# Kernel tuning notes

Hardware: AMD Instinct MI355X
Metric: run time of the kernel (lower is better)

The kernel has to match this reference:

```python
import jax, jax.numpy as jnp
import numpy as np

C = 96
HEADS = 6
WH, WW = 8, 8
N = WH * WW
EPS = 1e-5

def _rel_pos_index(wh, ww):
    ch, cw = np.meshgrid(np.arange(wh), np.arange(ww), indexing='ij')
    cf = np.stack([ch.reshape(-1), cw.reshape(-1)])  # [2, N]
    rel = (cf[:, :, None] - cf[:, None, :]).transpose(1, 2, 0)  # [N, N, 2]
    rel[..., 0] += wh - 1
    rel[..., 1] += ww - 1
    rel[..., 0] *= 2 * ww - 1
    return rel.sum(-1)  # [N, N]

REL_IDX = jnp.asarray(_rel_pos_index(WH, WW).reshape(-1))

def _shift_mask(H, W, wh, ww):
    # standard Swin shifted-window attention mask, values in {0, -100}
    sh, sw = wh // 2, ww // 2
    img = np.zeros((H, W))
    cnt = 0
    for hs in (slice(0, -wh), slice(-wh, -sh), slice(-sh, None)):
        for ws in (slice(0, -ww), slice(-ww, -sw), slice(-sw, None)):
            img[hs, ws] = cnt
            cnt += 1
    mw = img.reshape(H // wh, wh, W // ww, ww).transpose(0, 2, 1, 3).reshape(-1, wh * ww)
    diff = mw[:, None, :] - mw[:, :, None]
    return np.where(diff != 0, -100.0, 0.0).astype(np.float32)  # [nW, N, N]

def _partition(x):
    # [B, C, H, W] -> [B*nW, N, C], window index fastest within batch
    B, Cc, H, W = x.shape
    x = x.transpose(0, 2, 3, 1)
    x = x.reshape(B, H // WH, WH, W // WW, WW, Cc).transpose(0, 1, 3, 2, 4, 5)
    return x.reshape(-1, N, Cc)

def _merge(xw, B, H, W):
    Cc = xw.shape[-1]
    x = xw.reshape(B, H // WH, W // WW, WH, WW, Cc).transpose(0, 1, 3, 2, 4, 5)
    return x.reshape(B, H, W, Cc).transpose(0, 3, 1, 2)

def _ln(x, g, b):
    m = jnp.mean(x, -1, keepdims=True)
    v = jnp.mean((x - m) ** 2, -1, keepdims=True)
    return (x - m) / jnp.sqrt(v + EPS) * g + b

def _wsa(x, wqkv, bqkv, table, wproj, bproj, g, b, mask):
    B_, Nn, Cc = x.shape
    d = Cc // HEADS
    qkv = (x @ wqkv + bqkv).reshape(B_, Nn, 3, HEADS, d).transpose(2, 0, 3, 1, 4)
    q, k, v = qkv[0], qkv[1], qkv[2]
    bias = table[REL_IDX].reshape(Nn, Nn, HEADS).transpose(2, 0, 1)[None]  # [1,H,N,N]
    if mask is not None:
        nW = mask.shape[0]
        bias = bias + jnp.tile(mask, (B_ // nW, 1, 1))[:, None]  # [B_,1,N,N]
    scores = jnp.einsum('bhqd,bhkd->bhqk', q, k) * jnp.float32(1.0 / np.sqrt(d)) + bias
    attn = jax.nn.softmax(scores, axis=-1)
    out = jnp.einsum('bhqk,bhkd->bhqd', attn, v).transpose(0, 2, 1, 3).reshape(B_, Nn, Cc)
    out = out @ wproj + bproj
    return _ln(out + x, g, b)

def _ff(x, w1, b1, w2, b2, g, b):
    y = jax.nn.gelu(x @ w1 + b1, approximate=False) @ w2 + b2
    return _ln(y + x, g, b)

def setup_inputs() -> dict:
    key = jax.random.key(0)
    ks = jax.random.split(key, 20)
    B, H, W = 4, 192, 192
    inp = {'x': jax.random.normal(ks[0], (B, C, H, W), jnp.float32)}
    T = (2 * WH - 1) * (2 * WW - 1)
    def w(k, sh):
        return jax.random.normal(k, sh, jnp.float32) * 0.05
    i = 1
    for p in ('sa1', 'sa2'):
        inp[p + '_wqkv'] = w(ks[i], (C, 3 * C)); i += 1
        inp[p + '_bqkv'] = jnp.zeros((3 * C,), jnp.float32)
        inp[p + '_table'] = w(ks[i], (T, HEADS)); i += 1
        inp[p + '_wproj'] = w(ks[i], (C, C)); i += 1
        inp[p + '_bproj'] = jnp.zeros((C,), jnp.float32)
        inp[p + '_g'] = jnp.ones((C,), jnp.float32)
        inp[p + '_b'] = jnp.zeros((C,), jnp.float32)
    for p in ('ff1', 'ff2'):
        inp[p + '_w1'] = w(ks[i], (C, 2 * C)); i += 1
        inp[p + '_b1'] = jnp.zeros((2 * C,), jnp.float32)
        inp[p + '_w2'] = w(ks[i], (2 * C, C)); i += 1
        inp[p + '_b2'] = jnp.zeros((C,), jnp.float32)
        inp[p + '_g'] = jnp.ones((C,), jnp.float32)
        inp[p + '_b'] = jnp.zeros((C,), jnp.float32)
    return inp

def reference(x, sa1_wqkv, sa1_bqkv, sa1_table, sa1_wproj, sa1_bproj, sa1_g, sa1_b, ff1_w1, ff1_b1, ff1_w2, ff1_b2, ff1_g, ff1_b, sa2_wqkv, sa2_bqkv, sa2_table, sa2_wproj, sa2_bproj, sa2_g, sa2_b, ff2_w1, ff2_b1, ff2_w2, ff2_b2, ff2_g, ff2_b):
    B, Cc, H, W = x.shape
    mask = jnp.asarray(_shift_mask(H, W, WH, WW))
    xw = _partition(x)
    xw = _wsa(xw, sa1_wqkv, sa1_bqkv, sa1_table, sa1_wproj, sa1_bproj, sa1_g, sa1_b, None)
    xw = _ff(xw, ff1_w1, ff1_b1, ff1_w2, ff1_b2, ff1_g, ff1_b)
    x = _merge(xw, B, H, W)
    x = jnp.roll(x, (-(WH // 2), -(WW // 2)), axis=(2, 3))
    xw = _partition(x)
    xw = _wsa(xw, sa2_wqkv, sa2_bqkv, sa2_table, sa2_wproj, sa2_bproj, sa2_g, sa2_b, mask)
    xw = _ff(xw, ff2_w1, ff2_b1, ff2_w2, ff2_b2, ff2_g, ff2_b)
    x = _merge(xw, B, H, W)
    x = jnp.roll(x, (WH // 2, WW // 2), axis=(2, 3))
    return x
```

## Files before the change

kernel.cpp:

```cpp
#include <hip/hip_runtime.h>
#include <hip/hip_bf16.h>

typedef float  f32x4 __attribute__((ext_vector_type(4)));
typedef float  f32x2 __attribute__((ext_vector_type(2)));
typedef short  s16x4 __attribute__((ext_vector_type(4)));
typedef short  s16x8 __attribute__((ext_vector_type(8)));
typedef unsigned short u16;

#define DEVI __device__ __forceinline__
#define MFMA32(A,B,C) __builtin_amdgcn_mfma_f32_16x16x32_bf16(A,B,C,0,0,0)
#define MFMA16(A,B,C) __builtin_amdgcn_mfma_f32_16x16x16bf16_1k(A,B,C,0,0,0)

constexpr int NWD=24, WPI=576, NWIN=2304;
constexpr float LNEPS=1e-5f;
constexpr float LOG2E=1.4426950408889634f;

constexpr size_t PACK_STRIDE = 147456;
constexpr size_t BIAS1_OFF   = 294912;
constexpr size_t BIAS2_OFF   = 393216;
constexpr size_t XT_OFF      = 786432;
constexpr size_t WS1_OFF     = XT_OFF + 28311552;

constexpr int L_X  = 0;
constexpr int L_O  = 13312;
constexpr int L_RED= 26624;
constexpr int L_X2 = 0;
constexpr int L_Y1 = 13312;
constexpr int L_OUT= 13312;
constexpr int WSLICE = 38912;
constexpr int LTOT   = 2*WSLICE;

DEVI u16 f2b(float f){ union{float f;unsigned u;}v; v.f=f; unsigned r=v.u + 0x7FFFu + ((v.u>>16)&1u); return (u16)(r>>16); }
DEVI float b2f(u16 h){ union{unsigned u;float f;}v; v.u=((unsigned)h)<<16; return v.f; }

DEVI s16x4 pack4(f32x4 a){
  union{ __hip_bfloat16 b[4]; s16x4 s; } z;
  #pragma unroll
  for (int i=0;i<4;++i) z.b[i] = __hip_bfloat16(a[i]);
  return z.s;
}

DEVI float fexp2(float x){
#if __has_builtin(__builtin_amdgcn_exp2f)
  return __builtin_amdgcn_exp2f(x);
#else
  return exp2f(x);
#endif
}
DEVI float frcp(float x){
#if __has_builtin(__builtin_amdgcn_rcpf)
  return __builtin_amdgcn_rcpf(x);
#else
  return 1.f/x;
#endif
}

DEVI float gelu_f(float t){
  const float u2 = t*__builtin_fmaf(t*t, 0.1029433f, 2.3022083f);
  return t * frcp(1.f + fexp2(-u2));
}

__global__ void pack_gemm(const float* __restrict__ q1,const float* __restrict__ p1,
                          const float* __restrict__ a1,const float* __restrict__ c1,
                          const float* __restrict__ q2,const float* __restrict__ p2,
                          const float* __restrict__ a2,const float* __restrict__ c2,
                          char* __restrict__ ws){
  const int wv = (blockIdx.x*256 + threadIdx.x)>>6;
  const int lane = threadIdx.x & 63;
  const int stage = wv/144; const int t = wv%144;
  const float* src; int N, off, tl, nkt;
  if (t < 54)      { src = stage? q2:q1; N=288; off=0;      tl=t;     nkt=3; }
  else if (t < 72) { src = stage? p2:p1; N=96;  off=55296;  tl=t-54;  nkt=3; }
  else if (t <108) { src = stage? a2:a1; N=192; off=73728;  tl=t-72;  nkt=3; }
  else             { src = stage? c2:c1; N=96;  off=110592; tl=t-108; nkt=6; }
  const int kt = tl % nkt;
  const int k0 = kt*32 + (lane>>4)*8, n = (tl/nkt)*16 + (lane&15);
  u16 v[8];
  #pragma unroll
  for (int e=0;e<8;++e) v[e] = f2b(src[(k0+e)*N + n]);
  *(s16x8*)(ws + stage*PACK_STRIDE + off + tl*1024 + lane*16) = *(s16x8*)v;
}

__global__ void pack_bias(const float* __restrict__ t1, const float* __restrict__ t2,
                          char* __restrict__ ws){
  const int wv = (blockIdx.x*256 + threadIdx.x)>>6;
  const int lane = threadIdx.x & 63;
  const float* tb; float* dst; int hc=0, wc=0, head, til;
  if (wv < 96){ tb=t1; head=wv>>4; til=wv&15;
                dst=(float*)(ws + BIAS1_OFF + (size_t)((head*16+til)*64+lane)*16); }
  else { int r = wv-96; const int cls = r/96; r %= 96; head=r>>4; til=r&15;
         hc=cls>>1; wc=cls&1; tb=t2;
         dst=(float*)(ws + BIAS2_OFF + cls*98304 + (size_t)((head*16+til)*64+lane)*16); }
  const int mt=til>>2, nt=til&3;
  const int q = nt*16 + (lane&15); const int qi=q>>3, qj=q&7;
  const int rq = (hc?(qi<4?1:2):0)*3 + (wc?(qj<4?1:2):0);
  f32x4 o;
  #pragma unroll
  for (int r4=0;r4<4;++r4){
    const int kk = mt*16 + (lane>>4)*4 + r4; const int ki=kk>>3, kj=kk&7;
    float v = tb[((qi-ki+7)*15 + (qj-kj+7))*6 + head];
    const int rk = (hc?(ki<4?1:2):0)*3 + (wc?(kj<4?1:2):0);
    if (rq != rk) v -= 100.f;
    o[r4]=v*LOG2E;
  }
  *(f32x4*)dst = o;
}

__global__ __launch_bounds__(256) void to_tokens(const float* __restrict__ x, u16* __restrict__ xt){
  __shared__ u16 T[192*100];
  const int b = blockIdx.x/192, h = blockIdx.x%192;
  const int t = threadIdx.x;
  for (int i=t; i<4608; i+=256){
    const int c = i/48, w4 = (i%48)*4;
    const f32x4 v = *(const f32x4*)&x[((size_t)(b*96+c)*192+h)*192 + w4];
    #pragma unroll
    for (int e=0;e<4;++e) T[(w4+e)*100 + c] = f2b(v[e]);
  }
  __syncthreads();
  for (int i=t; i<2304; i+=256){
    const int tok = i/12, c8 = i%12;
    *(s16x8*)&xt[((size_t)(b*192+h)*192+tok)*96 + c8*8] = *(const s16x8*)&T[tok*100 + c8*8];
  }
}

template <int STAGE>
__global__ __launch_bounds__(768, 3) void swin_mfma(
    const u16* __restrict__ srcTok, u16* __restrict__ dstTok,
    const char* __restrict__ pack, const char* __restrict__ biasAll,
    const float* __restrict__ bqkv, const float* __restrict__ bproj,
    const float* __restrict__ g1v, const float* __restrict__ be1v,
    const float* __restrict__ b1v, const float* __restrict__ b2v,
    const float* __restrict__ g2v, const float* __restrict__ be2v)
{
  __shared__ f32x4 LDSv[LTOT/16];
  char* lds = (char*)LDSv;

  const int tid  = threadIdx.x;
  const int lane = tid & 63;
  const int wfl  = __builtin_amdgcn_readfirstlane(tid >> 6);
  const int wh   = wfl/6;
  const int hd   = wfl - 6*wh;
  const int g    = lane >> 4, li = lane & 15;
  const int win  = blockIdx.x*2 + wh;
  const int b    = win / WPI, wrem = win % WPI;
  const int whi  = wrem / NWD, wwi = wrem % NWD;
  char* ldsW     = lds + wh*WSLICE;
  constexpr int SH = (STAGE==2) ? 4 : 0;

  {
    const int wsel = (tid >= 384) ? 1 : 0;
    const int lt   = tid - wsel*384;
    const int winT = blockIdx.x*2 + wsel;
    const int bT   = winT / WPI, wremT = winT % WPI;
    const int h0T  = (wremT/NWD)*8, w0T = (wremT%NWD)*8;
    const int tok = lt/6, ch = lt%6;
    const int hh = (h0T + (tok>>3) + SH)%192, ww = (w0T + (tok&7) + SH)%192;
    const u16* sp = srcTok + ((size_t)(bT*192+hh)*192+ww)*96 + ch*16;
    char* ldsT = lds + wsel*WSLICE;
    *(s16x8*)(ldsT + L_X + tok*208 + ch*32)      = *(const s16x8*)sp;
    *(s16x8*)(ldsT + L_X + tok*208 + ch*32 + 16) = *(const s16x8*)(sp+8);
  }
  __syncthreads();

  s16x4 fq[4], fk[4], fv[4];
  {
    const float SCLQ = 0.25f*LOG2E;
    const f32x4 bqv = *(const f32x4*)(bqkv +      16*hd + 4*g);
    const f32x4 bkv = *(const f32x4*)(bqkv +  96 + 16*hd + 4*g);
    const float bvv = bqkv[192 + 16*hd + li];
    #pragma unroll
    for (int nt=0;nt<4;++nt){
      asm volatile("" ::: "memory");
      f32x4 aq=f32x4{0,0,0,0}, ak=f32x4{0,0,0,0}, av=f32x4{0,0,0,0};
      #pragma unroll
      for (int kt=0;kt<3;++kt){
        const s16x8 wqf = *(const s16x8*)(pack + ((   hd)*3+kt)*1024 + lane*16);
        const s16x8 wkf = *(const s16x8*)(pack + (( 6+hd)*3+kt)*1024 + lane*16);
        const s16x8 wvf = *(const s16x8*)(pack + ((12+hd)*3+kt)*1024 + lane*16);
        const s16x8 xf  = *(const s16x8*)(ldsW + L_X + (16*nt+li)*208 + kt*64 + g*16);
        aq = MFMA32(wqf, xf, aq);
        ak = MFMA32(wkf, xf, ak);
        av = MFMA32(xf, wvf, av);
      }
      f32x4 tq, tk, tv;
      #pragma unroll
      for (int r=0;r<4;++r){
        tq[r] = (aq[r]+bqv[r])*SCLQ;
        tk[r] =  ak[r]+bkv[r];
        tv[r] =  av[r]+bvv;
      }
      fq[nt]=pack4(tq); fk[nt]=pack4(tk); fv[nt]=pack4(tv);
    }
  }

  {
    const char* bb = biasAll;
    if (STAGE==2) bb += (size_t)(((whi==23)?2:0) + ((wwi==23)?1:0)) * 98304;
    #pragma unroll
    for (int nt=0;nt<4;++nt){
      f32x4 sc[4];
      #pragma unroll
      for (int mt=0;mt<4;++mt)
        sc[mt] = *(const f32x4*)(bb + (size_t)((hd*16 + mt*4+nt)*64 + lane)*16);
      #pragma unroll
      for (int mt=0;mt<4;++mt)
        sc[mt] = MFMA16(fk[mt], fq[nt], sc[mt]);
      float m = sc[0][0];
      #pragma unroll
      for (int mt=0;mt<4;++mt)
        #pragma unroll
        for (int r=0;r<4;++r) m = fmaxf(m, sc[mt][r]);
      m = fmaxf(m, __shfl_xor(m,16)); m = fmaxf(m, __shfl_xor(m,32));
      float s = 0.f; s16x4 pb[4];
      #pragma unroll
      for (int mt=0;mt<4;++mt){
        f32x4 pv;
        #pragma unroll
        for (int r=0;r<4;++r){ pv[r] = fexp2(sc[mt][r]-m); s += pv[r]; }
        pb[mt] = pack4(pv);
      }
      s += __shfl_xor(s,16); s += __shfl_xor(s,32);
      const float rs = frcp(s);
      f32x4 oa = f32x4{0,0,0,0};
      #pragma unroll
      for (int kt=0;kt<4;++kt)
        oa = MFMA16(fv[kt], pb[kt], oa);
      f32x4 ov;
      #pragma unroll
      for (int r=0;r<4;++r) ov[r] = oa[r]*rs;
      *(s16x4*)(ldsW + L_O + (16*nt+li)*208 + (16*hd+4*g)*2) = pack4(ov);
    }
  }
  __syncthreads();

  float z[4][4];
  {
    const f32x4 bpv = *(const f32x4*)(bproj + 16*hd + 4*g);
    f32x4 pa[4];
    #pragma unroll
    for (int nt=0;nt<4;++nt) pa[nt]=bpv;
    #pragma unroll
    for (int kt=0;kt<3;++kt){
      const s16x8 wpf = *(const s16x8*)(pack + 55296 + (hd*3+kt)*1024 + lane*16);
      #pragma unroll
      for (int nt=0;nt<4;++nt){
        const s16x8 of = *(const s16x8*)(ldsW + L_O + (16*nt+li)*208 + kt*64 + g*16);
        pa[nt] = MFMA32(wpf, of, pa[nt]);
      }
    }
    #pragma unroll
    for (int nt=0;nt<4;++nt){
      const s16x4 xr = *(const s16x4*)(ldsW + L_X + (16*nt+li)*208 + (16*hd+4*g)*2);
      #pragma unroll
      for (int r=0;r<4;++r) z[nt][r] = pa[nt][r] + b2f((u16)xr[r]);
    }
    #pragma unroll
    for (int nt=0;nt<4;++nt){
      float s1 = z[nt][0]+z[nt][1]+z[nt][2]+z[nt][3];
      float s2 = z[nt][0]*z[nt][0]+z[nt][1]*z[nt][1]+z[nt][2]*z[nt][2]+z[nt][3]*z[nt][3];
      s1 += __shfl_xor(s1,16); s1 += __shfl_xor(s1,32);
      s2 += __shfl_xor(s2,16); s2 += __shfl_xor(s2,32);
      if (lane < 16)
        *(f32x2*)(ldsW + L_RED + (hd*64 + nt*16 + li)*8) = f32x2{s1,s2};
    }
  }
  __syncthreads();
  {
    const f32x4 gv = *(const f32x4*)(g1v + 16*hd + 4*g);
    const f32x4 bv = *(const f32x4*)(be1v + 16*hd + 4*g);
    #pragma unroll
    for (int nt=0;nt<4;++nt){
      float su=0.f, sq=0.f;
      #pragma unroll
      for (int v=0;v<6;++v){
        const f32x2 p = *(const f32x2*)(ldsW + L_RED + (v*64 + nt*16 + li)*8);
        su += p[0]; sq += p[1];
      }
      const float mu = su*(1.f/96.f);
      const float rstd = rsqrtf(sq*(1.f/96.f) - mu*mu + LNEPS);
      f32x4 xo;
      #pragma unroll
      for (int r=0;r<4;++r) xo[r] = (z[nt][r]-mu)*rstd*gv[r] + bv[r];
      *(s16x4*)(ldsW + L_X2 + (16*nt+li)*208 + (16*hd+4*g)*2) = pack4(xo);
    }
  }
  __syncthreads();

  {
    f32x4 ya[2][4];
    #pragma unroll
    for (int jn=0;jn<2;++jn){
      const f32x4 b1f = *(const f32x4*)(b1v + 16*(hd+6*jn) + 4*g);
      #pragma unroll
      for (int nt=0;nt<4;++nt) ya[jn][nt]=b1f;
    }
    #pragma unroll
    for (int kt=0;kt<3;++kt){
      const s16x8 w1f0 = *(const s16x8*)(pack + 73728 + ((hd  )*3+kt)*1024 + lane*16);
      const s16x8 w1f1 = *(const s16x8*)(pack + 73728 + ((hd+6)*3+kt)*1024 + lane*16);
      #pragma unroll
      for (int nt=0;nt<4;++nt){
        const s16x8 xf = *(const s16x8*)(ldsW + L_X2 + (16*nt+li)*208 + kt*64 + g*16);
        ya[0][nt] = MFMA32(w1f0, xf, ya[0][nt]);
        ya[1][nt] = MFMA32(w1f1, xf, ya[1][nt]);
      }
    }
    #pragma unroll
    for (int jn=0;jn<2;++jn)
      #pragma unroll
      for (int nt=0;nt<4;++nt){
        f32x4 yo;
        #pragma unroll
        for (int r=0;r<4;++r) yo[r] = gelu_f(ya[jn][nt][r]);
        *(s16x4*)(ldsW + L_Y1 + (16*nt+li)*400 + (16*(hd+6*jn)+4*g)*2) = pack4(yo);
      }
  }
  __syncthreads();

  float z2[4][4]; float s1v[4], s2v[4];
  {
    const f32x4 b2f4 = *(const f32x4*)(b2v + 16*hd + 4*g);
    f32x4 fa[4];
    #pragma unroll
    for (int nt=0;nt<4;++nt) fa[nt]=b2f4;
    #pragma unroll
    for (int kt=0;kt<6;++kt){
      const s16x8 w2f = *(const s16x8*)(pack + 110592 + (hd*6+kt)*1024 + lane*16);
      #pragma unroll
      for (int nt=0;nt<4;++nt){
        const s16x8 yf = *(const s16x8*)(ldsW + L_Y1 + (16*nt+li)*400 + kt*64 + g*16);
        fa[nt] = MFMA32(w2f, yf, fa[nt]);
      }
    }
    #pragma unroll
    for (int nt=0;nt<4;++nt){
      const s16x4 xr = *(const s16x4*)(ldsW + L_X2 + (16*nt+li)*208 + (16*hd+4*g)*2);
      #pragma unroll
      for (int r=0;r<4;++r) z2[nt][r] = fa[nt][r] + b2f((u16)xr[r]);
    }
    #pragma unroll
    for (int nt=0;nt<4;++nt){
      float s1 = z2[nt][0]+z2[nt][1]+z2[nt][2]+z2[nt][3];
      float s2 = z2[nt][0]*z2[nt][0]+z2[nt][1]*z2[nt][1]+z2[nt][2]*z2[nt][2]+z2[nt][3]*z2[nt][3];
      s1 += __shfl_xor(s1,16); s1 += __shfl_xor(s1,32);
      s2 += __shfl_xor(s2,16); s2 += __shfl_xor(s2,32);
      s1v[nt]=s1; s2v[nt]=s2;
    }
  }
  __syncthreads();
  if (lane < 16){
    #pragma unroll
    for (int nt=0;nt<4;++nt)
      *(f32x2*)(ldsW + L_RED + (hd*64 + nt*16 + li)*8) = f32x2{s1v[nt],s2v[nt]};
  }
  __syncthreads();
  {
    const f32x4 gv = *(const f32x4*)(g2v + 16*hd + 4*g);
    const f32x4 bv = *(const f32x4*)(be2v + 16*hd + 4*g);
    #pragma unroll
    for (int nt=0;nt<4;++nt){
      float su=0.f, sq=0.f;
      #pragma unroll
      for (int v=0;v<6;++v){
        const f32x2 p = *(const f32x2*)(ldsW + L_RED + (v*64 + nt*16 + li)*8);
        su += p[0]; sq += p[1];
      }
      const float mu = su*(1.f/96.f);
      const float rstd = rsqrtf(sq*(1.f/96.f) - mu*mu + LNEPS);
      f32x4 oo;
      #pragma unroll
      for (int r=0;r<4;++r) oo[r] = (z2[nt][r]-mu)*rstd*gv[r] + bv[r];
      *(s16x4*)(ldsW + L_OUT + (16*nt+li)*208 + (16*hd+4*g)*2) = pack4(oo);
    }
  }
  __syncthreads();
  {
    const int wsel = (tid >= 384) ? 1 : 0;
    const int lt   = tid - wsel*384;
    const int winT = blockIdx.x*2 + wsel;
    const int bT   = winT / WPI, wremT = winT % WPI;
    const int h0T  = (wremT/NWD)*8, w0T = (wremT%NWD)*8;
    const int tok = lt/6, ch = lt%6;
    const int hh = (h0T + (tok>>3) + SH)%192, ww = (w0T + (tok&7) + SH)%192;
    char* ldsT = lds + wsel*WSLICE;
    u16* dp = dstTok + ((size_t)(bT*192+hh)*192+ww)*96 + ch*16;
    *(s16x8*)dp     = *(const s16x8*)(ldsT + L_OUT + tok*208 + ch*32);
    *(s16x8*)(dp+8) = *(const s16x8*)(ldsT + L_OUT + tok*208 + ch*32 + 16);
  }
}

__global__ __launch_bounds__(256) void untranspose(const u16* __restrict__ ws2, float* __restrict__ out){
  __shared__ u16 T[192*100];
  const int b = blockIdx.x / 192, ho = blockIdx.x % 192;
  const u16* row = ws2 + (size_t)(b*192 + ho)*192*96;
  const int t = threadIdx.x;
  for (int i = t; i < 2304; i += 256){
    const s16x8 v = *(const s16x8*)(row + i*8);
    const int wv = i/12, c8 = i%12;
    *(s16x8*)&T[wv*100 + c8*8] = v;
  }
  __syncthreads();
  #pragma unroll
  for (int j = 0; j < 18; ++j){
    const int flat = t + 256*j;
    const int c = flat/48, w4 = (flat%48)*4;
    f32x4 o;
    #pragma unroll
    for (int e=0;e<4;++e)
      o[e] = b2f(T[(w4+e)*100 + c]);
    *(f32x4*)&out[((size_t)(b*96 + c)*192 + ho)*192 + w4] = o;
  }
}

extern "C" void kernel_launch(void* const* d_in, const int* in_sizes, int n_in,
                              void* d_out, int out_size, void* d_ws, size_t ws_size,
                              hipStream_t stream) {
  const float* x       = (const float*)d_in[0];
  const float* s1_wqkv = (const float*)d_in[1];
  const float* s1_bqkv = (const float*)d_in[2];
  const float* s1_tbl  = (const float*)d_in[3];
  const float* s1_wp   = (const float*)d_in[4];
  const float* s1_bp   = (const float*)d_in[5];
  const float* s1_g    = (const float*)d_in[6];
  const float* s1_b    = (const float*)d_in[7];
  const float* s2_wqkv = (const float*)d_in[8];
  const float* s2_bqkv = (const float*)d_in[9];
  const float* s2_tbl  = (const float*)d_in[10];
  const float* s2_wp   = (const float*)d_in[11];
  const float* s2_bp   = (const float*)d_in[12];
  const float* s2_g    = (const float*)d_in[13];
  const float* s2_b    = (const float*)d_in[14];
  const float* f1_w1   = (const float*)d_in[15];
  const float* f1_b1   = (const float*)d_in[16];
  const float* f1_w2   = (const float*)d_in[17];
  const float* f1_b2   = (const float*)d_in[18];
  const float* f1_g    = (const float*)d_in[19];
  const float* f1_b    = (const float*)d_in[20];
  const float* f2_w1   = (const float*)d_in[21];
  const float* f2_b1   = (const float*)d_in[22];
  const float* f2_w2   = (const float*)d_in[23];
  const float* f2_b2   = (const float*)d_in[24];
  const float* f2_g    = (const float*)d_in[25];
  const float* f2_b    = (const float*)d_in[26];

  char* ws  = (char*)d_ws;
  u16* regionA = (u16*)(ws + XT_OFF);
  u16* ws1     = (u16*)(ws + WS1_OFF);

  pack_gemm<<<72, 256, 0, stream>>>(s1_wqkv, s1_wp, f1_w1, f1_w2,
                                    s2_wqkv, s2_wp, f2_w1, f2_w2, ws);
  pack_bias<<<120, 256, 0, stream>>>(s1_tbl, s2_tbl, ws);
  to_tokens<<<4*192, 256, 0, stream>>>(x, regionA);

  swin_mfma<1><<<NWIN/2, 768, 0, stream>>>(regionA, ws1,
      ws, ws + BIAS1_OFF,
      s1_bqkv, s1_bp, s1_g, s1_b, f1_b1, f1_b2, f1_g, f1_b);
  swin_mfma<2><<<NWIN/2, 768, 0, stream>>>(ws1, regionA,
      ws + PACK_STRIDE, ws + BIAS2_OFF,
      s2_bqkv, s2_bp, s2_g, s2_b, f2_b1, f2_b2, f2_g, f2_b);

  untranspose<<<4*192, 256, 0, stream>>>(regionA, (float*)d_out);
}
```

Measured before the change: 191.1 us.

## Prefetch weight fragments before barriers and drop a sync via dedicated LDS reduction area

Weight fragments for the QKV, projection, FF1 and FF2 matmuls are now loaded into registers before each preceding barrier, so their global-memory latency overlaps the sync and the LDS writes. The QKV loop is reordered to keep all twelve accumulators live and interleave MFMAs across tiles. The layernorm reduction buffer moves to its own LDS region past the other buffers, which removes one __syncthreads in the second layernorm. The cost is higher register pressure and a larger LDS footprint per block, which could lower occupancy.

Result: no change. 188.0 us (-1.6%).

```diff
diff --git a/kernel.cpp b/kernel.cpp
--- a/kernel.cpp
+++ b/kernel.cpp
@@ -23,11 +23,11 @@
 
 constexpr int L_X  = 0;
 constexpr int L_O  = 13312;
-constexpr int L_RED= 26624;
 constexpr int L_X2 = 0;
 constexpr int L_Y1 = 13312;
 constexpr int L_OUT= 13312;
-constexpr int WSLICE = 38912;
+constexpr int L_RED= 38912;
+constexpr int WSLICE = 41984;
 constexpr int LTOT   = 2*WSLICE;
 
 DEVI u16 f2b(float f){ union{float f;unsigned u;}v; v.f=f; unsigned r=v.u + 0x7FFFu + ((v.u>>16)&1u); return (u16)(r>>16); }
@@ -160,34 +160,42 @@
     *(s16x8*)(ldsT + L_X + tok*208 + ch*32)      = *(const s16x8*)sp;
     *(s16x8*)(ldsT + L_X + tok*208 + ch*32 + 16) = *(const s16x8*)(sp+8);
   }
+  s16x8 wqf[3], wkf[3], wvf[3];
+  #pragma unroll
+  for (int kt=0;kt<3;++kt){
+    wqf[kt] = *(const s16x8*)(pack + ((   hd)*3+kt)*1024 + lane*16);
+    wkf[kt] = *(const s16x8*)(pack + (( 6+hd)*3+kt)*1024 + lane*16);
+    wvf[kt] = *(const s16x8*)(pack + ((12+hd)*3+kt)*1024 + lane*16);
+  }
   __syncthreads();
 
   s16x4 fq[4], fk[4], fv[4];
   {
+    f32x4 aq[4], ak[4], av[4];
+    #pragma unroll
+    for (int nt=0;nt<4;++nt){ aq[nt]=f32x4{0,0,0,0}; ak[nt]=f32x4{0,0,0,0}; av[nt]=f32x4{0,0,0,0}; }
+    #pragma unroll
+    for (int kt=0;kt<3;++kt){
+      #pragma unroll
+      for (int nt=0;nt<4;++nt){
+        const s16x8 xf = *(const s16x8*)(ldsW + L_X + (16*nt+li)*208 + kt*64 + g*16);
+        aq[nt] = MFMA32(wqf[kt], xf, aq[nt]);
+        ak[nt] = MFMA32(wkf[kt], xf, ak[nt]);
+        av[nt] = MFMA32(xf, wvf[kt], av[nt]);
+      }
+    }
     const float SCLQ = 0.25f*LOG2E;
     const f32x4 bqv = *(const f32x4*)(bqkv +      16*hd + 4*g);
     const f32x4 bkv = *(const f32x4*)(bqkv +  96 + 16*hd + 4*g);
     const float bvv = bqkv[192 + 16*hd + li];
     #pragma unroll
     for (int nt=0;nt<4;++nt){
-      asm volatile("" ::: "memory");
-      f32x4 aq=f32x4{0,0,0,0}, ak=f32x4{0,0,0,0}, av=f32x4{0,0,0,0};
-      #pragma unroll
-      for (int kt=0;kt<3;++kt){
-        const s16x8 wqf = *(const s16x8*)(pack + ((   hd)*3+kt)*1024 + lane*16);
-        const s16x8 wkf = *(const s16x8*)(pack + (( 6+hd)*3+kt)*1024 + lane*16);
-        const s16x8 wvf = *(const s16x8*)(pack + ((12+hd)*3+kt)*1024 + lane*16);
-        const s16x8 xf  = *(const s16x8*)(ldsW + L_X + (16*nt+li)*208 + kt*64 + g*16);
-        aq = MFMA32(wqf, xf, aq);
-        ak = MFMA32(wkf, xf, ak);
-        av = MFMA32(xf, wvf, av);
-      }
       f32x4 tq, tk, tv;
       #pragma unroll
       for (int r=0;r<4;++r){
-        tq[r] = (aq[r]+bqv[r])*SCLQ;
-        tk[r] =  ak[r]+bkv[r];
-        tv[r] =  av[r]+bvv;
+        tq[r] = (aq[nt][r]+bqv[r])*SCLQ;
+        tk[r] =  ak[nt][r]+bkv[r];
+        tv[r] =  av[nt][r]+bvv;
       }
       fq[nt]=pack4(tq); fk[nt]=pack4(tk); fv[nt]=pack4(tv);
     }
@@ -231,6 +239,10 @@
       *(s16x4*)(ldsW + L_O + (16*nt+li)*208 + (16*hd+4*g)*2) = pack4(ov);
     }
   }
+  s16x8 wpf[3];
+  #pragma unroll
+  for (int kt=0;kt<3;++kt)
+    wpf[kt] = *(const s16x8*)(pack + 55296 + (hd*3+kt)*1024 + lane*16);
   __syncthreads();
 
   float z[4][4];
@@ -241,11 +253,10 @@
     for (int nt=0;nt<4;++nt) pa[nt]=bpv;
     #pragma unroll
     for (int kt=0;kt<3;++kt){
-      const s16x8 wpf = *(const s16x8*)(pack + 55296 + (hd*3+kt)*1024 + lane*16);
       #pragma unroll
       for (int nt=0;nt<4;++nt){
         const s16x8 of = *(const s16x8*)(ldsW + L_O + (16*nt+li)*208 + kt*64 + g*16);
-        pa[nt] = MFMA32(wpf, of, pa[nt]);
+        pa[nt] = MFMA32(wpf[kt], of, pa[nt]);
       }
     }
     #pragma unroll
@@ -284,6 +295,12 @@
       *(s16x4*)(ldsW + L_X2 + (16*nt+li)*208 + (16*hd+4*g)*2) = pack4(xo);
     }
   }
+  s16x8 w1f[2][3];
+  #pragma unroll
+  for (int kt=0;kt<3;++kt){
+    w1f[0][kt] = *(const s16x8*)(pack + 73728 + ((hd  )*3+kt)*1024 + lane*16);
+    w1f[1][kt] = *(const s16x8*)(pack + 73728 + ((hd+6)*3+kt)*1024 + lane*16);
+  }
   __syncthreads();
 
   {
@@ -296,13 +313,11 @@
     }
     #pragma unroll
     for (int kt=0;kt<3;++kt){
-      const s16x8 w1f0 = *(const s16x8*)(pack + 73728 + ((hd  )*3+kt)*1024 + lane*16);
-      const s16x8 w1f1 = *(const s16x8*)(pack + 73728 + ((hd+6)*3+kt)*1024 + lane*16);
       #pragma unroll
       for (int nt=0;nt<4;++nt){
         const s16x8 xf = *(const s16x8*)(ldsW + L_X2 + (16*nt+li)*208 + kt*64 + g*16);
-        ya[0][nt] = MFMA32(w1f0, xf, ya[0][nt]);
-        ya[1][nt] = MFMA32(w1f1, xf, ya[1][nt]);
+        ya[0][nt] = MFMA32(w1f[0][kt], xf, ya[0][nt]);
+        ya[1][nt] = MFMA32(w1f[1][kt], xf, ya[1][nt]);
       }
     }
     #pragma unroll
@@ -315,9 +330,13 @@
         *(s16x4*)(ldsW + L_Y1 + (16*nt+li)*400 + (16*(hd+6*jn)+4*g)*2) = pack4(yo);
       }
   }
-  __syncthreads();
-
-  float z2[4][4]; float s1v[4], s2v[4];
+  s16x8 w2f[6];
+  #pragma unroll
+  for (int kt=0;kt<6;++kt)
+    w2f[kt] = *(const s16x8*)(pack + 110592 + (hd*6+kt)*1024 + lane*16);
+  __syncthreads();
+
+  float z2[4][4];
   {
     const f32x4 b2f4 = *(const f32x4*)(b2v + 16*hd + 4*g);
     f32x4 fa[4];
@@ -325,11 +344,10 @@
     for (int nt=0;nt<4;++nt) fa[nt]=b2f4;
     #pragma unroll
     for (int kt=0;kt<6;++kt){
-      const s16x8 w2f = *(const s16x8*)(pack + 110592 + (hd*6+kt)*1024 + lane*16);
       #pragma unroll
       for (int nt=0;nt<4;++nt){
         const s16x8 yf = *(const s16x8*)(ldsW + L_Y1 + (16*nt+li)*400 + kt*64 + g*16);
-        fa[nt] = MFMA32(w2f, yf, fa[nt]);
+        fa[nt] = MFMA32(w2f[kt], yf, fa[nt]);
       }
     }
     #pragma unroll
@@ -344,14 +362,9 @@
       float s2 = z2[nt][0]*z2[nt][0]+z2[nt][1]*z2[nt][1]+z2[nt][2]*z2[nt][2]+z2[nt][3]*z2[nt][3];
       s1 += __shfl_xor(s1,16); s1 += __shfl_xor(s1,32);
       s2 += __shfl_xor(s2,16); s2 += __shfl_xor(s2,32);
-      s1v[nt]=s1; s2v[nt]=s2;
-    }
-  }
-  __syncthreads();
-  if (lane < 16){
-    #pragma unroll
-    for (int nt=0;nt<4;++nt)
-      *(f32x2*)(ldsW + L_RED + (hd*64 + nt*16 + li)*8) = f32x2{s1v[nt],s2v[nt]};
+      if (lane < 16)
+        *(f32x2*)(ldsW + L_RED + (hd*64 + nt*16 + li)*8) = f32x2{s1,s2};
+    }
   }
   __syncthreads();
   {
```
